# Kernel optimization log

Hardware: AMD Instinct MI355X
Metric: run time of the kernel (lower is better)

## Reference

```python
import jax, jax.numpy as jnp
import numpy as np

B, T, K, H = 4, 2048, 128, 8
MASK = True


def setup_inputs() -> dict:
    key = jax.random.key(0)
    ks = jax.random.split(key, 6)
    s = 0.02
    return {
        "x": jax.random.normal(ks[0], (B, T, K), dtype=jnp.float32),
        "Wq": jax.random.normal(ks[1], (K, H * K), dtype=jnp.float32) * s,
        "Wk": jax.random.normal(ks[2], (K, H * K), dtype=jnp.float32) * s,
        "Wv": jax.random.normal(ks[3], (K, H * K), dtype=jnp.float32) * s,
        "Wu": jax.random.normal(ks[4], (H * K, K), dtype=jnp.float32) * s,
        "bu": jnp.zeros((K,), dtype=jnp.float32),
    }


def reference(x, Wq, Wk, Wv, Wu, bu):
    b, t, k = x.shape
    h = H
    q = (x @ Wq).reshape(b, t, h, k)
    kk = (x @ Wk).reshape(b, t, h, k)
    # module pre-scales values by k**-0.25 (idiosyncratic but faithful)
    v = (x @ Wv).reshape(b, t, h, k) * (k ** -0.25)
    # scores [b, h, t, t], scaled by k**-0.5
    scores = jnp.einsum('bthd,bshd->bhts', q, kk) * (k ** -0.5)
    if MASK:
        causal = jnp.tril(jnp.ones((t, t), dtype=bool))
        scores = jnp.where(causal, scores, -jnp.inf)
    w = jax.nn.softmax(scores, axis=-1)
    out = jnp.einsum('bhts,bshd->bthd', w, v).reshape(b, t, h * k)
    return out @ Wu + bu
```

## Files before the change

kernel.cpp:

```cpp
#include <hip/hip_runtime.h>
#include <hip/hip_bf16.h>
#include <math.h>

#define B_ 4
#define T_ 2048
#define D_ 128
#define H_ 8
#define BT_ 8192
#define HD_ 1024

typedef __attribute__((ext_vector_type(8))) short bf16x8;
typedef __attribute__((ext_vector_type(4))) float f32x4;

__device__ __forceinline__ short f2bf(float f) {
  union { float f; unsigned u; } v; v.f = f;
  return (short)((v.u + 0x8000u) >> 16);
}

#if __has_builtin(__builtin_amdgcn_exp2f)
#define EXP2F(x) __builtin_amdgcn_exp2f(x)
#else
#define EXP2F(x) exp2f(x)
#endif

#define QSCALE 0.12752040242046492f
#define VSCALE 0.29730177875068026f

__device__ __forceinline__ void gld16(const short* g, short* l) {
  __builtin_amdgcn_global_load_lds(
      (const __attribute__((address_space(1))) void*)g,
      (__attribute__((address_space(3))) void*)l, 16, 0, 0);
}

__global__ __launch_bounds__(256) void prep(
    const float* __restrict__ x, const float* __restrict__ Wq,
    const float* __restrict__ Wk, const float* __restrict__ Wv,
    short* __restrict__ xbf, short* __restrict__ WT)
{
  __shared__ __align__(16) short Tt[128*128];
  const int tid = threadIdx.x;
  const int id = blockIdx.x;
  if (id < 24) {
    const int wsel = id >> 3, nt = id & 7;
    const float* W = (wsel == 0) ? Wq : (wsel == 1) ? Wk : Wv;
    #pragma unroll 4
    for (int i = tid; i < 4096; i += 256) {
      int k = i >> 5, n4 = (i & 31) << 2;
      float4 v = *(const float4*)&W[(size_t)k * HD_ + nt*128 + n4];
      float vv[4] = {v.x, v.y, v.z, v.w};
      #pragma unroll
      for (int j = 0; j < 4; j++) {
        int n = n4 + j;
        Tt[n*128 + (((k >> 3) ^ (n & 15)) << 3) + (k & 7)] = f2bf(vv[j]);
      }
    }
    __syncthreads();
    short* dst = WT + (size_t)id * 16384;
    #pragma unroll 2
    for (int i = tid; i < 2048; i += 256)
      *(bf16x8*)&dst[i*8] = *(bf16x8*)&Tt[i*8];
  } else {
    const int xb = id - 24;
    const float* xs = x + (size_t)xb * 16384;
    short* dst = xbf + (size_t)xb * 16384;
    #pragma unroll 4
    for (int i = tid; i < 4096; i += 256) {
      float4 v = ((const float4*)xs)[i];
      int row = i >> 5, c = (i & 31) >> 1, half = i & 1;
      short4 p;
      p.x = f2bf(v.x); p.y = f2bf(v.y); p.z = f2bf(v.z); p.w = f2bf(v.w);
      *(short4*)&dst[(row*16 + (c ^ (row & 15)))*8 + half*4] = p;
    }
  }
}

__global__ __launch_bounds__(256, 2) void qkv_proj(
    const short* __restrict__ xbf, const short* __restrict__ WT,
    short* __restrict__ Qw, short* __restrict__ Kw, short* __restrict__ Vw)
{
  __shared__ __align__(16) short As[16384];
  __shared__ __align__(16) short Bs[16384];
  const int tid = threadIdx.x;
  const int w = tid >> 6, lane = tid & 63, quad = lane >> 4, l16 = lane & 15;
  const int m0 = blockIdx.x * 128;

  {
    const short* asrc = xbf + (size_t)blockIdx.x * 16384;
    const short* bsrc = WT + (size_t)blockIdx.y * 16384;
    const int so = w*4096 + lane*8;
    #pragma unroll
    for (int cc = 0; cc < 8; cc++) {
      gld16(asrc + so + cc*512, &As[w*4096 + cc*512]);
      gld16(bsrc + so + cc*512, &Bs[w*4096 + cc*512]);
    }
  }
  __syncthreads();

  const int wsel = (int)blockIdx.y >> 3;
  const int rA0 = (w & 1) * 64, rB0 = (w >> 1) * 64;
  const short* RA = (wsel <= 1) ? Bs : As;
  const short* RB = (wsel <= 1) ? As : Bs;

  f32x4 acc[4][4];
  #pragma unroll
  for (int a = 0; a < 4; a++)
    #pragma unroll
    for (int b = 0; b < 4; b++) acc[a][b] = (f32x4){0.f, 0.f, 0.f, 0.f};

  #pragma unroll
  for (int kk = 0; kk < 4; kk++) {
    const int swz = ((kk*4 + quad) ^ l16) << 3;
    bf16x8 af[4], bfv[4];
    #pragma unroll
    for (int ai = 0; ai < 4; ai++) af[ai]  = *(const bf16x8*)&RA[(rA0 + ai*16 + l16)*128 + swz];
    #pragma unroll
    for (int bi = 0; bi < 4; bi++) bfv[bi] = *(const bf16x8*)&RB[(rB0 + bi*16 + l16)*128 + swz];
    #pragma unroll
    for (int ai = 0; ai < 4; ai++)
      #pragma unroll
      for (int bi = 0; bi < 4; bi++)
        acc[ai][bi] = __builtin_amdgcn_mfma_f32_16x16x32_bf16(af[ai], bfv[bi], acc[ai][bi], 0, 0, 0);
  }

  __syncthreads();
  if (wsel <= 1) {
    const float sc = wsel ? 1.0f : QSCALE;
    #pragma unroll
    for (int ai = 0; ai < 4; ai++) {
      #pragma unroll
      for (int bi = 0; bi < 4; bi++) {
        const int d0 = rA0 + ai*16 + quad*4;
        const int t  = rB0 + bi*16 + l16;
        const int tile = t >> 6, tl = t & 63;
        short4 p;
        p.x = f2bf(acc[ai][bi][0] * sc);
        p.y = f2bf(acc[ai][bi][1] * sc);
        p.z = f2bf(acc[ai][bi][2] * sc);
        p.w = f2bf(acc[ai][bi][3] * sc);
        *(short4*)&As[tile*8192 + tl*128 + (((d0 >> 3) ^ (tl & 15)) << 3) + (d0 & 7)] = p;
      }
    }
  } else {
    #pragma unroll
    for (int ai = 0; ai < 4; ai++) {
      #pragma unroll
      for (int bi = 0; bi < 4; bi++) {
        const int t0 = rA0 + ai*16 + quad*4;
        const int d  = rB0 + bi*16 + l16;
        const int tile = t0 >> 6, tl0 = t0 & 63;
        short4 p;
        p.x = f2bf(acc[ai][bi][0] * VSCALE);
        p.y = f2bf(acc[ai][bi][1] * VSCALE);
        p.z = f2bf(acc[ai][bi][2] * VSCALE);
        p.w = f2bf(acc[ai][bi][3] * VSCALE);
        *(short4*)&As[tile*8192 + d*64 + (((tl0 >> 3) ^ (d & 7)) << 3) + (tl0 & 7)] = p;
      }
    }
  }
  __syncthreads();

  const int h = (int)blockIdx.y & 7;
  const int b = m0 >> 11, t0 = m0 & 2047;
  short* base = ((wsel == 0) ? Qw : (wsel == 1) ? Kw : Vw)
              + (size_t)(b*H_ + h)*262144 + (size_t)t0*128;
  #pragma unroll 2
  for (int i = tid; i < 2048; i += 256)
    *(bf16x8*)&base[i*8] = *(bf16x8*)&As[i*8];
}

__global__ __launch_bounds__(256, 4) void attn_kernel(
    const short* __restrict__ Qw, const short* __restrict__ Kw,
    const short* __restrict__ Vw, short* __restrict__ attnw)
{
  __shared__ __align__(16) short Ks[8192];
  __shared__ __align__(16) short Vs[8192];
  __shared__ __align__(16) short Ps[4096];

  const int tid = threadIdx.x;
  const int id = (int)blockIdx.x;
  const int xcd = id & 7;
  const int j   = id >> 3;
  const int u   = j & 3;
  const int q   = (j >> 2) & 7;
  const int vv  = (j >> 5) & 3;
  const int slot = u ^ vv;
  const int qi = (slot == 0) ? q : (slot == 1) ? 15 - q
               : (slot == 2) ? 16 + q : 31 - q;
  const int bh = xcd | (u << 3);
  const int b = bh >> 3, h = bh & 7;
  const int w = tid >> 6, lane = tid & 63, quad = lane >> 4, l16 = lane & 15;
  const int rowQ = qi*64 + w*16;

  const short* Qp = Qw + (size_t)bh * 262144;
  const short* Kp = Kw + (size_t)bh * 262144;
  const short* Vp = Vw + (size_t)bh * 262144;

  bf16x8 qa[4];
  {
    const int tl = (rowQ & 63) + l16;
    const short* qp = Qp + ((size_t)(rowQ >> 6) << 13) + tl*128;
    #pragma unroll
    for (int kk = 0; kk < 4; kk++)
      qa[kk] = *(const bf16x8*)(qp + (((kk*4 + quad) ^ (tl & 15)) << 3));
  }

  f32x4 o[8];
  #pragma unroll
  for (int e = 0; e < 8; e++) o[e] = (f32x4){0,0,0,0};
  float l[4] = {0,0,0,0};

  short* Pw = &Ps[w*1024];
  const int so = w*2048 + lane*8;
  const int nIter = qi + 1;

  for (int it = 0; it < nIter; ++it) {
    if (it) __syncthreads();
    {
      const short* kt = Kp + ((size_t)it << 13);
      const short* vt = Vp + ((size_t)it << 13);
      #pragma unroll
      for (int cc = 0; cc < 4; cc++) {
        gld16(kt + so + cc*512, &Ks[w*2048 + cc*512]);
        gld16(vt + so + cc*512, &Vs[w*2048 + cc*512]);
      }
    }
    __syncthreads();

    f32x4 s[4];
    #pragma unroll
    for (int nj = 0; nj < 4; nj++) s[nj] = (f32x4){0,0,0,0};
    #pragma unroll
    for (int kk = 0; kk < 4; kk++) {
      const int swz = ((kk*4 + quad) ^ l16) << 3;
      #pragma unroll
      for (int nj = 0; nj < 4; nj++) {
        bf16x8 kb = *(const bf16x8*)&Ks[(nj*16 + l16)*128 + swz];
        s[nj] = __builtin_amdgcn_mfma_f32_16x16x32_bf16(qa[kk], kb, s[nj], 0, 0, 0);
      }
    }

    if (it < qi) {
      #pragma unroll
      for (int nj = 0; nj < 4; nj++) {
        #pragma unroll
        for (int r = 0; r < 4; r++) {
          float p = EXP2F(s[nj][r]);
          l[r] += p;
          const int row = quad*4 + r, col = nj*16 + l16;
          Pw[row*64 + (((col >> 3) ^ (row & 7)) << 3) + (col & 7)] = f2bf(p);
        }
      }
    } else {
      const int s0 = it * 64;
      #pragma unroll
      for (int nj = 0; nj < 4; nj++) {
        const int key = s0 + nj*16 + l16;
        #pragma unroll
        for (int r = 0; r < 4; r++) {
          float p = (key > rowQ + quad*4 + r) ? 0.f : EXP2F(s[nj][r]);
          l[r] += p;
          const int row = quad*4 + r, col = nj*16 + l16;
          Pw[row*64 + (((col >> 3) ^ (row & 7)) << 3) + (col & 7)] = f2bf(p);
        }
      }
    }

    #pragma unroll
    for (int kk2 = 0; kk2 < 2; kk2++) {
      const int swz = ((kk2*4 + quad) ^ (l16 & 7)) << 3;
      bf16x8 pa = *(bf16x8*)&Pw[l16*64 + swz];
      #pragma unroll
      for (int e = 0; e < 8; e++) {
        bf16x8 vb = *(const bf16x8*)&Vs[(e*16 + l16)*64 + swz];
        o[e] = __builtin_amdgcn_mfma_f32_16x16x32_bf16(pa, vb, o[e], 0, 0, 0);
      }
    }
  }

  #pragma unroll
  for (int r = 0; r < 4; r++) {
    float t = l[r];
    t += __shfl_xor(t, 1); t += __shfl_xor(t, 2);
    t += __shfl_xor(t, 4); t += __shfl_xor(t, 8);
    l[r] = 1.0f / t;
  }
  __syncthreads();
  #pragma unroll
  for (int e = 0; e < 8; e++) {
    const int c = e*2 + (l16 >> 3);
    #pragma unroll
    for (int r = 0; r < 4; r++) {
      const int lrow = w*16 + quad*4 + r;
      const int sub = lrow >> 5, r32 = lrow & 31;
      Ks[sub*4096 + r32*128 + ((c ^ (r32 & 15)) << 3) + (l16 & 7)] =
          f2bf(o[e][r] * l[r]);
    }
  }
  __syncthreads();
  const int st0 = b*64 + qi*2;
  #pragma unroll 2
  for (int i = tid; i < 1024; i += 256) {
    const int sub = i >> 9, rem = i & 511;
    short* dst = attnw + ((size_t)(st0 + sub)*8 + h)*4096 + rem*8;
    *(bf16x8*)dst = *(const bf16x8*)&Ks[i*8];
  }
}

__global__ __launch_bounds__(256) void wu_prep(
    const float* __restrict__ Wu, short* __restrict__ WuT)
{
  __shared__ __align__(16) short Tt[128*128];
  const int tid = threadIdx.x;
  const int kc = blockIdx.x;
  #pragma unroll 4
  for (int i = tid; i < 4096; i += 256) {
    int kl = i >> 5, n4 = (i & 31) << 2;
    float4 v = *(const float4*)&Wu[(size_t)(kc*128 + kl) * D_ + n4];
    float vv[4] = {v.x, v.y, v.z, v.w};
    #pragma unroll
    for (int j = 0; j < 4; j++) {
      int n = n4 + j;
      Tt[n*128 + (((kl >> 3) ^ (n & 15)) << 3) + (kl & 7)] = f2bf(vv[j]);
    }
  }
  __syncthreads();
  short* dst = WuT + (size_t)kc * 16384;
  #pragma unroll 2
  for (int i = tid; i < 2048; i += 256)
    *(bf16x8*)&dst[i*8] = *(bf16x8*)&Tt[i*8];
}

__global__ __launch_bounds__(256, 2) void out_proj(
    const short* __restrict__ attnw, const short* __restrict__ WuT,
    const float* __restrict__ bu, float* __restrict__ out)
{
  __shared__ __align__(16) short As2[2][2048];
  __shared__ __align__(16) short Bs2[2][16384];
  const int tid = threadIdx.x;
  const int w = tid >> 6, lane = tid & 63, quad = lane >> 4, l16 = lane & 15;
  const int m0 = (int)blockIdx.x * 16;
  const int mtile32 = m0 >> 5, half = (m0 >> 4) & 1;

  f32x4 o2[2];
  o2[0] = (f32x4){0,0,0,0}; o2[1] = (f32x4){0,0,0,0};

  {
    const short* ab = attnw + (size_t)(mtile32*8)*4096 + half*2048;
    gld16(ab + w*512 + lane*8, &As2[0][w*512]);
    #pragma unroll
    for (int cc = 0; cc < 8; cc++)
      gld16(WuT + w*4096 + cc*512 + lane*8, &Bs2[0][w*4096 + cc*512]);
  }
  int buf = 0;

  for (int kc = 0; kc < 8; kc++) {
    __syncthreads();
    if (kc < 7) {
      const short* ab = attnw + (size_t)(mtile32*8 + kc + 1)*4096 + half*2048;
      const short* bb = WuT + (size_t)(kc + 1)*16384;
      gld16(ab + w*512 + lane*8, &As2[buf^1][w*512]);
      #pragma unroll
      for (int cc = 0; cc < 8; cc++)
        gld16(bb + w*4096 + cc*512 + lane*8, &Bs2[buf^1][w*4096 + cc*512]);
    }
    const short* as = &As2[buf][0];
    const short* bs = &Bs2[buf][0];
    #pragma unroll
    for (int kk = 0; kk < 4; kk++) {
      const int swz = ((kk*4 + quad) ^ l16) << 3;
      bf16x8 a = *(const bf16x8*)&as[l16*128 + swz];
      #pragma unroll
      for (int e = 0; e < 2; e++) {
        bf16x8 bfr = *(const bf16x8*)&bs[((w*2 + e)*16 + l16)*128 + swz];
        o2[e] = __builtin_amdgcn_mfma_f32_16x16x32_bf16(a, bfr, o2[e], 0, 0, 0);
      }
    }
    buf ^= 1;
  }

  #pragma unroll
  for (int e = 0; e < 2; e++) {
    const int n = (w*2 + e)*16 + l16;
    const float bias = bu[n];
    #pragma unroll
    for (int r = 0; r < 4; r++) {
      const int mm = m0 + quad*4 + r;
      out[(size_t)mm*D_ + n] = o2[e][r] + bias;
    }
  }
}

extern "C" void kernel_launch(void* const* d_in, const int* in_sizes, int n_in,
                              void* d_out, int out_size, void* d_ws, size_t ws_size,
                              hipStream_t stream) {
  (void)in_sizes; (void)n_in; (void)out_size; (void)ws_size;
  const float* x  = (const float*)d_in[0];
  const float* Wq = (const float*)d_in[1];
  const float* Wk = (const float*)d_in[2];
  const float* Wv = (const float*)d_in[3];
  const float* Wu = (const float*)d_in[4];
  const float* bu = (const float*)d_in[5];
  float* out = (float*)d_out;

  const size_t headElems = (size_t)B_ * H_ * T_ * D_;
  short* Qw    = (short*)d_ws;
  short* Kw    = Qw + headElems;
  short* Vw    = Kw + headElems;
  short* attnw = Vw + headElems;
  short* xbf = attnw;
  short* WT  = attnw + 1048576;
  short* WuT = Kw;

  prep<<<dim3(88), 256, 0, stream>>>(x, Wq, Wk, Wv, xbf, WT);
  qkv_proj<<<dim3(64, 24), 256, 0, stream>>>(xbf, WT, Qw, Kw, Vw);
  attn_kernel<<<dim3(1024), 256, 0, stream>>>(Qw, Kw, Vw, attnw);
  wu_prep<<<dim3(8), 256, 0, stream>>>(Wu, WuT);
  out_proj<<<dim3(512), 256, 0, stream>>>(attnw, WuT, bu, out);
}
```

Baseline: 159.2 us.

## Fuse Wu transpose into prep and compute Q/K/V per block reusing x tile

The qkv projection now launches one block per (row tile, head) and loops over Q, K and V inside the block, keeping the x tile in LDS and reloading only the weight tile between passes. This cuts redundant x loads and the grid size from 1536 to 512 blocks. Output staging moves to the B buffer so x stays resident. Separately, when the workspace is large enough, the Wu bf16 transpose is folded into the prep kernel using extra blocks, removing one launch. The cost is less parallelism in qkv_proj and serialized weight reloads inside each block.

```diff
diff --git a/kernel.cpp b/kernel.cpp
--- a/kernel.cpp
+++ b/kernel.cpp
@@ -32,10 +32,33 @@
       (__attribute__((address_space(3))) void*)l, 16, 0, 0);
 }
 
+__device__ __forceinline__ void wu_transpose_body(
+    const float* __restrict__ Wu, short* __restrict__ WuT,
+    short* Tt, int kc, int tid)
+{
+  #pragma unroll 4
+  for (int i = tid; i < 4096; i += 256) {
+    int kl = i >> 5, n4 = (i & 31) << 2;
+    float4 v = *(const float4*)&Wu[(size_t)(kc*128 + kl) * D_ + n4];
+    float vv[4] = {v.x, v.y, v.z, v.w};
+    #pragma unroll
+    for (int j = 0; j < 4; j++) {
+      int n = n4 + j;
+      Tt[n*128 + (((kl >> 3) ^ (n & 15)) << 3) + (kl & 7)] = f2bf(vv[j]);
+    }
+  }
+  __syncthreads();
+  short* dst = WuT + (size_t)kc * 16384;
+  #pragma unroll 2
+  for (int i = tid; i < 2048; i += 256)
+    *(bf16x8*)&dst[i*8] = *(bf16x8*)&Tt[i*8];
+}
+
 __global__ __launch_bounds__(256) void prep(
     const float* __restrict__ x, const float* __restrict__ Wq,
     const float* __restrict__ Wk, const float* __restrict__ Wv,
-    short* __restrict__ xbf, short* __restrict__ WT)
+    const float* __restrict__ Wu,
+    short* __restrict__ xbf, short* __restrict__ WT, short* __restrict__ WuT)
 {
   __shared__ __align__(16) short Tt[128*128];
   const int tid = threadIdx.x;
@@ -59,7 +82,7 @@
     #pragma unroll 2
     for (int i = tid; i < 2048; i += 256)
       *(bf16x8*)&dst[i*8] = *(bf16x8*)&Tt[i*8];
-  } else {
+  } else if (id < 88) {
     const int xb = id - 24;
     const float* xs = x + (size_t)xb * 16384;
     short* dst = xbf + (size_t)xb * 16384;
@@ -71,6 +94,8 @@
       p.x = f2bf(v.x); p.y = f2bf(v.y); p.z = f2bf(v.z); p.w = f2bf(v.w);
       *(short4*)&dst[(row*16 + (c ^ (row & 15)))*8 + half*4] = p;
     }
+  } else {
+    wu_transpose_body(Wu, WuT, Tt, id - 88, tid);
   }
 }
 
@@ -82,90 +107,102 @@
   __shared__ __align__(16) short Bs[16384];
   const int tid = threadIdx.x;
   const int w = tid >> 6, lane = tid & 63, quad = lane >> 4, l16 = lane & 15;
-  const int m0 = blockIdx.x * 128;
+  const int m0 = (int)blockIdx.x * 128;
+  const int head = (int)blockIdx.y;
+  const int so = w*4096 + lane*8;
 
   {
     const short* asrc = xbf + (size_t)blockIdx.x * 16384;
-    const short* bsrc = WT + (size_t)blockIdx.y * 16384;
-    const int so = w*4096 + lane*8;
+    const short* bsrc = WT + (size_t)head * 16384;
     #pragma unroll
     for (int cc = 0; cc < 8; cc++) {
       gld16(asrc + so + cc*512, &As[w*4096 + cc*512]);
       gld16(bsrc + so + cc*512, &Bs[w*4096 + cc*512]);
     }
   }
-  __syncthreads();
-
-  const int wsel = (int)blockIdx.y >> 3;
+
   const int rA0 = (w & 1) * 64, rB0 = (w >> 1) * 64;
-  const short* RA = (wsel <= 1) ? Bs : As;
-  const short* RB = (wsel <= 1) ? As : Bs;
-
-  f32x4 acc[4][4];
-  #pragma unroll
-  for (int a = 0; a < 4; a++)
-    #pragma unroll
-    for (int b = 0; b < 4; b++) acc[a][b] = (f32x4){0.f, 0.f, 0.f, 0.f};
-
-  #pragma unroll
-  for (int kk = 0; kk < 4; kk++) {
-    const int swz = ((kk*4 + quad) ^ l16) << 3;
-    bf16x8 af[4], bfv[4];
-    #pragma unroll
-    for (int ai = 0; ai < 4; ai++) af[ai]  = *(const bf16x8*)&RA[(rA0 + ai*16 + l16)*128 + swz];
-    #pragma unroll
-    for (int bi = 0; bi < 4; bi++) bfv[bi] = *(const bf16x8*)&RB[(rB0 + bi*16 + l16)*128 + swz];
-    #pragma unroll
-    for (int ai = 0; ai < 4; ai++)
-      #pragma unroll
-      for (int bi = 0; bi < 4; bi++)
-        acc[ai][bi] = __builtin_amdgcn_mfma_f32_16x16x32_bf16(af[ai], bfv[bi], acc[ai][bi], 0, 0, 0);
-  }
-
-  __syncthreads();
-  if (wsel <= 1) {
-    const float sc = wsel ? 1.0f : QSCALE;
-    #pragma unroll
-    for (int ai = 0; ai < 4; ai++) {
-      #pragma unroll
-      for (int bi = 0; bi < 4; bi++) {
-        const int d0 = rA0 + ai*16 + quad*4;
-        const int t  = rB0 + bi*16 + l16;
-        const int tile = t >> 6, tl = t & 63;
-        short4 p;
-        p.x = f2bf(acc[ai][bi][0] * sc);
-        p.y = f2bf(acc[ai][bi][1] * sc);
-        p.z = f2bf(acc[ai][bi][2] * sc);
-        p.w = f2bf(acc[ai][bi][3] * sc);
-        *(short4*)&As[tile*8192 + tl*128 + (((d0 >> 3) ^ (tl & 15)) << 3) + (d0 & 7)] = p;
-      }
-    }
-  } else {
-    #pragma unroll
-    for (int ai = 0; ai < 4; ai++) {
-      #pragma unroll
-      for (int bi = 0; bi < 4; bi++) {
-        const int t0 = rA0 + ai*16 + quad*4;
-        const int d  = rB0 + bi*16 + l16;
-        const int tile = t0 >> 6, tl0 = t0 & 63;
-        short4 p;
-        p.x = f2bf(acc[ai][bi][0] * VSCALE);
-        p.y = f2bf(acc[ai][bi][1] * VSCALE);
-        p.z = f2bf(acc[ai][bi][2] * VSCALE);
-        p.w = f2bf(acc[ai][bi][3] * VSCALE);
-        *(short4*)&As[tile*8192 + d*64 + (((tl0 >> 3) ^ (d & 7)) << 3) + (tl0 & 7)] = p;
-      }
-    }
-  }
-  __syncthreads();
-
-  const int h = (int)blockIdx.y & 7;
-  const int b = m0 >> 11, t0 = m0 & 2047;
-  short* base = ((wsel == 0) ? Qw : (wsel == 1) ? Kw : Vw)
-              + (size_t)(b*H_ + h)*262144 + (size_t)t0*128;
-  #pragma unroll 2
-  for (int i = tid; i < 2048; i += 256)
-    *(bf16x8*)&base[i*8] = *(bf16x8*)&As[i*8];
+  const int b = m0 >> 11, t0g = m0 & 2047;
+  const int h = head;
+
+  #pragma unroll 1
+  for (int wsel = 0; wsel < 3; wsel++) {
+    __syncthreads();
+    const short* RA = (wsel <= 1) ? Bs : As;
+    const short* RB = (wsel <= 1) ? As : Bs;
+
+    f32x4 acc[4][4];
+    #pragma unroll
+    for (int a = 0; a < 4; a++)
+      #pragma unroll
+      for (int bb = 0; bb < 4; bb++) acc[a][bb] = (f32x4){0.f, 0.f, 0.f, 0.f};
+
+    #pragma unroll
+    for (int kk = 0; kk < 4; kk++) {
+      const int swz = ((kk*4 + quad) ^ l16) << 3;
+      bf16x8 af[4], bfv[4];
+      #pragma unroll
+      for (int ai = 0; ai < 4; ai++) af[ai]  = *(const bf16x8*)&RA[(rA0 + ai*16 + l16)*128 + swz];
+      #pragma unroll
+      for (int bi = 0; bi < 4; bi++) bfv[bi] = *(const bf16x8*)&RB[(rB0 + bi*16 + l16)*128 + swz];
+      #pragma unroll
+      for (int ai = 0; ai < 4; ai++)
+        #pragma unroll
+        for (int bi = 0; bi < 4; bi++)
+          acc[ai][bi] = __builtin_amdgcn_mfma_f32_16x16x32_bf16(af[ai], bfv[bi], acc[ai][bi], 0, 0, 0);
+    }
+
+    __syncthreads();
+    if (wsel <= 1) {
+      const float sc = wsel ? 1.0f : QSCALE;
+      #pragma unroll
+      for (int ai = 0; ai < 4; ai++) {
+        #pragma unroll
+        for (int bi = 0; bi < 4; bi++) {
+          const int d0 = rA0 + ai*16 + quad*4;
+          const int t  = rB0 + bi*16 + l16;
+          const int tile = t >> 6, tl = t & 63;
+          short4 p;
+          p.x = f2bf(acc[ai][bi][0] * sc);
+          p.y = f2bf(acc[ai][bi][1] * sc);
+          p.z = f2bf(acc[ai][bi][2] * sc);
+          p.w = f2bf(acc[ai][bi][3] * sc);
+          *(short4*)&Bs[tile*8192 + tl*128 + (((d0 >> 3) ^ (tl & 15)) << 3) + (d0 & 7)] = p;
+        }
+      }
+    } else {
+      #pragma unroll
+      for (int ai = 0; ai < 4; ai++) {
+        #pragma unroll
+        for (int bi = 0; bi < 4; bi++) {
+          const int t0 = rA0 + ai*16 + quad*4;
+          const int d  = rB0 + bi*16 + l16;
+          const int tile = t0 >> 6, tl0 = t0 & 63;
+          short4 p;
+          p.x = f2bf(acc[ai][bi][0] * VSCALE);
+          p.y = f2bf(acc[ai][bi][1] * VSCALE);
+          p.z = f2bf(acc[ai][bi][2] * VSCALE);
+          p.w = f2bf(acc[ai][bi][3] * VSCALE);
+          *(short4*)&Bs[tile*8192 + d*64 + (((tl0 >> 3) ^ (d & 7)) << 3) + (tl0 & 7)] = p;
+        }
+      }
+    }
+    __syncthreads();
+
+    short* base = ((wsel == 0) ? Qw : (wsel == 1) ? Kw : Vw)
+                + (size_t)(b*H_ + h)*262144 + (size_t)t0g*128;
+    #pragma unroll 2
+    for (int i = tid; i < 2048; i += 256)
+      *(bf16x8*)&base[i*8] = *(bf16x8*)&Bs[i*8];
+
+    if (wsel < 2) {
+      __syncthreads();
+      const short* bsrc = WT + (size_t)((wsel + 1)*8 + head) * 16384;
+      #pragma unroll
+      for (int cc = 0; cc < 8; cc++)
+        gld16(bsrc + so + cc*512, &Bs[w*4096 + cc*512]);
+    }
+  }
 }
 
 __global__ __launch_bounds__(256, 4) void attn_kernel(
@@ -310,24 +347,7 @@
     const float* __restrict__ Wu, short* __restrict__ WuT)
 {
   __shared__ __align__(16) short Tt[128*128];
-  const int tid = threadIdx.x;
-  const int kc = blockIdx.x;
-  #pragma unroll 4
-  for (int i = tid; i < 4096; i += 256) {
-    int kl = i >> 5, n4 = (i & 31) << 2;
-    float4 v = *(const float4*)&Wu[(size_t)(kc*128 + kl) * D_ + n4];
-    float vv[4] = {v.x, v.y, v.z, v.w};
-    #pragma unroll
-    for (int j = 0; j < 4; j++) {
-      int n = n4 + j;
-      Tt[n*128 + (((kl >> 3) ^ (n & 15)) << 3) + (kl & 7)] = f2bf(vv[j]);
-    }
-  }
-  __syncthreads();
-  short* dst = WuT + (size_t)kc * 16384;
-  #pragma unroll 2
-  for (int i = tid; i < 2048; i += 256)
-    *(bf16x8*)&dst[i*8] = *(bf16x8*)&Tt[i*8];
+  wu_transpose_body(Wu, WuT, Tt, blockIdx.x, threadIdx.x);
 }
 
 __global__ __launch_bounds__(256, 2) void out_proj(
@@ -393,7 +413,7 @@
 extern "C" void kernel_launch(void* const* d_in, const int* in_sizes, int n_in,
                               void* d_out, int out_size, void* d_ws, size_t ws_size,
                               hipStream_t stream) {
-  (void)in_sizes; (void)n_in; (void)out_size; (void)ws_size;
+  (void)in_sizes; (void)n_in; (void)out_size;
   const float* x  = (const float*)d_in[0];
   const float* Wq = (const float*)d_in[1];
   const float* Wk = (const float*)d_in[2];
@@ -409,11 +429,13 @@
   short* attnw = Vw + headElems;
   short* xbf = attnw;
   short* WT  = attnw + 1048576;
-  short* WuT = Kw;
-
-  prep<<<dim3(88), 256, 0, stream>>>(x, Wq, Wk, Wv, xbf, WT);
-  qkv_proj<<<dim3(64, 24), 256, 0, stream>>>(xbf, WT, Qw, Kw, Vw);
+
+  const bool extraWu = ws_size >= (64ull << 20) + (1ull << 20);
+  short* WuT = extraWu ? (short*)((char*)d_ws + (64ull << 20)) : Kw;
+
+  prep<<<dim3(extraWu ? 96 : 88), 256, 0, stream>>>(x, Wq, Wk, Wv, Wu, xbf, WT, WuT);
+  qkv_proj<<<dim3(64, 8), 256, 0, stream>>>(xbf, WT, Qw, Kw, Vw);
   attn_kernel<<<dim3(1024), 256, 0, stream>>>(Qw, Kw, Vw, attnw);
-  wu_prep<<<dim3(8), 256, 0, stream>>>(Wu, WuT);
+  if (!extraWu) wu_prep<<<dim3(8), 256, 0, stream>>>(Wu, WuT);
   out_proj<<<dim3(512), 256, 0, stream>>>(attnw, WuT, bu, out);
 }
```

Measured after the change: 152.8 us. 1.04x faster.
